# Optimization experiments

Measured on AMD Instinct MI355X. Metric: run time of the kernel, lower is better.

## Reference

```python
import jax, jax.numpy as jnp
import numpy as np
import itertools, functools, operator

NUM_RBF = 32
CUTOFF = 5.0
METRIC = (1, 1, 1)


def _count_bits(x):
    return bin(x).count("1")


def _sign_euclidean(a, b):
    a >>= 1
    s = 0
    while a:
        s += _count_bits(a & b)
        a >>= 1
    return 1 if (s & 1) == 0 else -1


def build_cayley(metric):
    """Dense [2^n, 2^n, 2^n] geometric multiplication (Cayley) table, shortlex blade order."""
    n = len(metric)
    blade_sets = itertools.chain.from_iterable(
        itertools.combinations([1 << i for i in range(n)], r) for r in range(n + 1)
    )
    index_to_bitmap = [functools.reduce(operator.or_, t, 0) for t in blade_sets]
    bitmap_to_index = {b: i for i, b in enumerate(index_to_bitmap)}
    N = 2 ** n
    cayley = np.zeros((N, N, N), dtype=np.float32)
    for i in range(N):
        bi = index_to_bitmap[i]
        for j in range(N):
            bj = index_to_bitmap[j]
            sign = _sign_euclidean(bi, bj)
            bm = bi & bj
            k = 0
            while bm:
                if bm & 1:
                    sign *= metric[k]
                k += 1
                bm >>= 1
            cayley[i, bitmap_to_index[bi ^ bj], j] = sign
    return cayley


CAYLEY = jnp.asarray(build_cayley(METRIC))  # [8,8,8], sparse +/-1 structure


def geometric_product(a, b):
    # torch: einsum('...i,ijk,...k->...j', a, cayley, b)
    return jnp.einsum('...i,ijk,...k->...j', a, CAYLEY, b)


def setup_inputs() -> dict:
    key = jax.random.key(0)
    k0, k1, k2, k3, k4, k5 = jax.random.split(key, 6)
    N, E, C = 50000, 800000, 16
    h = jax.random.normal(k0, (N, C, 8), jnp.float32)
    pos = jax.random.uniform(k1, (N, 3), jnp.float32) * 10.0
    edge_index = jax.random.randint(k2, (2, E), 0, N, jnp.int32)
    W_rbf = jax.random.normal(k3, (NUM_RBF, C), jnp.float32) / np.sqrt(NUM_RBF)
    W_out = jax.random.normal(k4, (C, C), jnp.float32) / np.sqrt(C)
    W_sgp = jax.random.normal(k5, (C, C), jnp.float32) / np.sqrt(C)
    return {"h": h, "pos": pos, "edge_index": edge_index,
            "W_rbf": W_rbf, "W_out": W_out, "W_sgp": W_sgp}


def reference(h, pos, edge_index, W_rbf, W_out, W_sgp):
    N, C, B = h.shape
    src, dst = edge_index[0], edge_index[1]

    # relative geometry
    rel = pos[dst] - pos[src]                                  # [E,3]
    dist = jnp.sqrt(jnp.sum(rel * rel, axis=-1) + 1e-12)       # [E]

    # embed unit relative vector as a grade-1 multivector (blades 1..3)
    rel_mv = jnp.zeros((rel.shape[0], 1, B), h.dtype)
    rel_mv = rel_mv.at[:, 0, 1:4].set(rel / dist[:, None])     # [E,1,8]

    # radial weights: gaussian smearing -> linear -> cosine cutoff envelope
    mus = jnp.linspace(0.0, CUTOFF, NUM_RBF, dtype=h.dtype)
    gamma = (NUM_RBF / CUTOFF) ** 2
    rbf = jnp.exp(-gamma * (dist[:, None] - mus) ** 2)         # [E,32]
    env = 0.5 * (jnp.cos(jnp.pi * dist / CUTOFF) + 1.0) * (dist < CUTOFF)
    w_e = (rbf @ W_rbf) * env[:, None]                          # [E,C]

    # equivariant messages: geometric product against edge multivector
    msg = geometric_product(h[src], rel_mv) * w_e[..., None]   # [E,C,8]
    agg = jax.ops.segment_sum(msg, dst, num_segments=N)        # [N,C,8]

    # MVLinear channel mixing (shared across blades)
    out = jnp.einsum('nci,co->noi', agg, W_out)                # [N,C,8]

    # MACE-style higher-order: steerable geometric product self-interaction
    q = jnp.einsum('nci,co->noi', h, W_sgp)                    # [N,C,8]
    return out + geometric_product(out, q)
```

## Files before the change

### kernel.cpp

```cpp
#include <hip/hip_runtime.h>

#define CUTOFF 5.0f
#define GAMMA 40.96f
#define MU_STEP 0.16129032f
#define INV_MU 6.2f
#define PI_F 3.14159265358979f
#define MAXDEG 64


__global__ __launch_bounds__(256) void k_fill_direct(
    const float* __restrict__ pos, const int* __restrict__ ei,
    int* __restrict__ deg, int* __restrict__ rec, int E)
{
    int e = blockIdx.x * 256 + threadIdx.x;
    if (e >= E) return;
    int src = ei[e], dst = ei[E + e];
    float dx = pos[dst*3+0] - pos[src*3+0];
    float dy = pos[dst*3+1] - pos[src*3+1];
    float dz = pos[dst*3+2] - pos[src*3+2];
    float d = sqrtf(dx*dx + dy*dy + dz*dz + 1e-12f);
    if (d < CUTOFF) {
        int slot = atomicAdd(&deg[dst], 1);
        if (slot < MAXDEG) rec[dst*MAXDEG + slot] = src;
    }
}

__global__ __launch_bounds__(256) void k_gather_finalize(
    const float* __restrict__ h, const float* __restrict__ pos,
    const int* __restrict__ rec, const int* __restrict__ deg,
    const float* __restrict__ Wrbf, const float* __restrict__ Wout,
    const float* __restrict__ Wsgp, float* __restrict__ out, int N)
{
    __shared__ float s_wr[512];
    __shared__ float s_Wout[256];
    __shared__ float s_Wsgp[256];
    __shared__ float s_agg[16*132];
    __shared__ float s_h[16*132];

    const int t  = threadIdx.x;
    const int nl = t >> 4;
    const int c  = t & 15;
    const int lane  = t & 63;
    const int gbase = lane & 48;
    const long long nodeBase = (long long)blockIdx.x * 16;
    const long long n = nodeBase + nl;

    s_wr[t]       = Wrbf[t];
    s_wr[t + 256] = Wrbf[t + 256];
    s_Wout[t] = Wout[t];
    s_Wsgp[t] = Wsgp[t];

    for (int idx = t; idx < 512; idx += 256) {
        int nn = idx >> 5;
        int r  = idx & 31;
        long long node = nodeBase + nn;
        float4 vh = make_float4(0,0,0,0);
        if (node < N) vh = *(const float4*)(h + node*128 + (long long)r*4);
        *(float4*)(&s_h[nn*132 + r*4]) = vh;
    }
    __syncthreads();

    float m0=0,m1=0,m2=0,m3=0,m4=0,m5=0,m6=0,m7=0;
    if (n < N) {
        const float px = pos[n*3+0], py = pos[n*3+1], pz = pos[n*3+2];
        const int start = (int)n * MAXDEG;
        const int dg    = min(deg[n], MAXDEG);
        for (int base = 0; base < dg; base += 2) {
            const int i1ok = (base + 1 < dg) ? 1 : 0;
            const int s0 = rec[start + base];
            const int s1 = rec[start + base + i1ok];

            const float4* hp0 = (const float4*)(h + (((long long)s0*16 + c) << 3));
            const float4* hp1 = (const float4*)(h + (((long long)s1*16 + c) << 3));
            const float4 A0 = hp0[0], B0 = hp0[1];
            const float4 A1 = hp1[0], B1 = hp1[1];

            const float dx0 = px - pos[s0*3+0];
            const float dy0 = py - pos[s0*3+1];
            const float dz0 = pz - pos[s0*3+2];
            const float dx1 = px - pos[s1*3+0];
            const float dy1 = py - pos[s1*3+1];
            const float dz1 = pz - pos[s1*3+2];

            const float d0 = sqrtf(dx0*dx0 + dy0*dy0 + dz0*dz0 + 1e-12f);
            const float d1 = sqrtf(dx1*dx1 + dy1*dy1 + dz1*dz1 + 1e-12f);
            const float inv0 = 1.0f / d0, inv1 = 1.0f / d1;
            const float ux0 = dx0*inv0, uy0 = dy0*inv0, uz0 = dz0*inv0;
            const float ux1 = dx1*inv1, uy1 = dy1*inv1, uz1 = dz1*inv1;
            const float env0 = 0.5f * (__cosf(PI_F * d0 * (1.0f/CUTOFF)) + 1.0f);
            const float env1 = 0.5f * (__cosf(PI_F * d1 * (1.0f/CUTOFF)) + 1.0f);

            const int kl0 = min(max(0, __float2int_rn(d0 * INV_MU) - 3), 25);
            const int kl1 = min(max(0, __float2int_rn(d1 * INV_MU) - 3), 25);

            const int   sel   = c >> 3;
            const float dsel  = sel ? d1 : d0;
            const int   klsel = sel ? kl1 : kl0;
            const float xx = dsel - MU_STEP * (float)(klsel + (c & 7));
            const float ee = __expf(-GAMMA * xx * xx);

            float w0 = 0.0f, w1 = 0.0f;
            #pragma unroll
            for (int j = 0; j < 7; ++j) {
                const float e0 = __shfl(ee, gbase + j);
                const float e1 = __shfl(ee, gbase + 8 + j);
                w0 += e0 * s_wr[(kl0 + j)*16 + c];
                w1 += e1 * s_wr[(kl1 + j)*16 + c];
            }
            w0 *= env0;
            w1 *= env1 * (float)i1ok;

            m0 += (A0.y*ux0 + A0.z*uy0 + A0.w*uz0) * w0 + (A1.y*ux1 + A1.z*uy1 + A1.w*uz1) * w1;
            m1 += (A0.x*ux0 + B0.x*uy0 + B0.y*uz0) * w0 + (A1.x*ux1 + B1.x*uy1 + B1.y*uz1) * w1;
            m2 += (A0.x*uy0 - B0.x*ux0 + B0.z*uz0) * w0 + (A1.x*uy1 - B1.x*ux1 + B1.z*uz1) * w1;
            m3 += (A0.x*uz0 - B0.y*ux0 - B0.z*uy0) * w0 + (A1.x*uz1 - B1.y*ux1 - B1.z*uy1) * w1;
            m4 += (A0.y*uy0 - A0.z*ux0 + B0.w*uz0) * w0 + (A1.y*uy1 - A1.z*ux1 + B1.w*uz1) * w1;
            m5 += (A0.y*uz0 - A0.w*ux0 - B0.w*uy0) * w0 + (A1.y*uz1 - A1.w*ux1 - B1.w*uy1) * w1;
            m6 += (A0.z*uz0 - A0.w*uy0 + B0.w*ux0) * w0 + (A1.z*uz1 - A1.w*uy1 + B1.w*ux1) * w1;
            m7 += (B0.z*ux0 - B0.y*uy0 + B0.x*uz0) * w0 + (B1.z*ux1 - B1.y*uy1 + B1.x*uz1) * w1;
        }
    }

    __syncthreads();
    float* ag = &s_agg[nl*132 + c*8];
    *(float4*)(ag)     = make_float4(m0, m1, m2, m3);
    *(float4*)(ag + 4) = make_float4(m4, m5, m6, m7);
    __syncthreads();

    const int o = c;
    const float* A = &s_agg[nl*132];
    const float* H = &s_h[nl*132];

    float o0=0,o1=0,o2=0,o3=0,o4=0,o5=0,o6=0,o7=0;
    float q0=0,q1=0,q2=0,q3=0,q4=0,q5=0,q6=0,q7=0;
    #pragma unroll
    for (int cc = 0; cc < 16; ++cc) {
        const float wo = s_Wout[cc*16 + o];
        const float ws = s_Wsgp[cc*16 + o];
        const float* a  = A + cc*8;
        const float* hh = H + cc*8;
        o0 += a[0]*wo; o1 += a[1]*wo; o2 += a[2]*wo; o3 += a[3]*wo;
        o4 += a[4]*wo; o5 += a[5]*wo; o6 += a[6]*wo; o7 += a[7]*wo;
        q0 += hh[0]*ws; q1 += hh[1]*ws; q2 += hh[2]*ws; q3 += hh[3]*ws;
        q4 += hh[4]*ws; q5 += hh[5]*ws; q6 += hh[6]*ws; q7 += hh[7]*ws;
    }

    const float r0 = o0 + (o0*q0 + o1*q1 + o2*q2 + o3*q3 - o4*q4 - o5*q5 - o6*q6 - o7*q7);
    const float r1 = o1 + (o0*q1 + o1*q0 - o2*q4 - o3*q5 + o4*q2 + o5*q3 - o6*q7 - o7*q6);
    const float r2 = o2 + (o0*q2 + o1*q4 + o2*q0 - o3*q6 - o4*q1 + o5*q7 + o6*q3 + o7*q5);
    const float r3 = o3 + (o0*q3 + o1*q5 + o2*q6 + o3*q0 - o4*q7 - o5*q1 - o6*q2 - o7*q4);
    const float r4 = o4 + (o0*q4 + o1*q2 - o2*q1 + o3*q7 + o4*q0 - o5*q6 + o6*q5 + o7*q3);
    const float r5 = o5 + (o0*q5 + o1*q3 - o2*q7 - o3*q1 + o4*q6 + o5*q0 - o6*q4 - o7*q2);
    const float r6 = o6 + (o0*q6 + o1*q7 + o2*q3 - o3*q2 - o4*q5 + o5*q4 + o6*q0 + o7*q1);
    const float r7 = o7 + (o0*q7 + o1*q6 - o2*q5 + o3*q4 + o4*q3 - o5*q2 + o6*q1 + o7*q0);

    if (n < N) {
        float* op = out + (n*16 + o)*8;
        *(float4*)(op)     = make_float4(r0, r1, r2, r3);
        *(float4*)(op + 4) = make_float4(r4, r5, r6, r7);
    }
}

extern "C" void kernel_launch(void* const* d_in, const int* in_sizes, int n_in,
                              void* d_out, int out_size, void* d_ws, size_t ws_size,
                              hipStream_t stream) {
    const float* h    = (const float*)d_in[0];
    const float* pos  = (const float*)d_in[1];
    const int*   ei   = (const int*)d_in[2];
    const float* Wrbf = (const float*)d_in[3];
    const float* Wout = (const float*)d_in[4];
    const float* Wsgp = (const float*)d_in[5];
    float* out = (float*)d_out;

    const int N = in_sizes[0] / 128;
    const int E = in_sizes[2] / 2;

    int* deg = (int*)d_ws;
    int* rec = deg + N;

    hipMemsetAsync(deg, 0, (size_t)N * sizeof(int), stream);

    const int eBlocks = (E + 255) / 256;
    k_fill_direct<<<eBlocks, 256, 0, stream>>>(pos, ei, deg, rec, E);

    const int gBlocks = (N + 15) / 16;
    k_gather_finalize<<<gBlocks, 256, 0, stream>>>(
        h, pos, rec, deg, Wrbf, Wout, Wsgp, out, N);
}
```

Before: 149.2 us.

## Fuse memset, edge bucketing and node gather into one cooperative persistent kernel

Replaces the memset plus two kernel launches with a single cooperative kernel that zeroes degrees, buckets edges by destination, then processes node tiles in a persistent loop, with grid-wide syncs between phases. The aim is to remove launch overhead and inter-kernel gaps. The cutoff test now compares squared distance and skips the sqrt. In exchange it adds grid.sync costs, caps the grid at the occupancy limit (hardcoded 256 CUs), and loops tiles persistently.

```diff
diff --git a/kernel.cpp b/kernel.cpp
--- a/kernel.cpp
+++ b/kernel.cpp
@@ -1,163 +1,171 @@
 #include <hip/hip_runtime.h>
+#include <hip/hip_cooperative_groups.h>
+
+namespace cg = cooperative_groups;
 
 #define CUTOFF 5.0f
+#define CUTOFF2 25.0f
 #define GAMMA 40.96f
 #define MU_STEP 0.16129032f
 #define INV_MU 6.2f
 #define PI_F 3.14159265358979f
 #define MAXDEG 64
 
-
-__global__ __launch_bounds__(256) void k_fill_direct(
-    const float* __restrict__ pos, const int* __restrict__ ei,
-    int* __restrict__ deg, int* __restrict__ rec, int E)
+__global__ __launch_bounds__(256) void k_fused(
+    const float* __restrict__ h, const float* __restrict__ pos,
+    const int* __restrict__ ei, const float* __restrict__ Wrbf,
+    const float* __restrict__ Wout, const float* __restrict__ Wsgp,
+    float* __restrict__ out, int* __restrict__ deg, int* __restrict__ rec,
+    int N, int E, int tiles)
 {
-    int e = blockIdx.x * 256 + threadIdx.x;
-    if (e >= E) return;
-    int src = ei[e], dst = ei[E + e];
-    float dx = pos[dst*3+0] - pos[src*3+0];
-    float dy = pos[dst*3+1] - pos[src*3+1];
-    float dz = pos[dst*3+2] - pos[src*3+2];
-    float d = sqrtf(dx*dx + dy*dy + dz*dz + 1e-12f);
-    if (d < CUTOFF) {
-        int slot = atomicAdd(&deg[dst], 1);
-        if (slot < MAXDEG) rec[dst*MAXDEG + slot] = src;
-    }
-}
-
-__global__ __launch_bounds__(256) void k_gather_finalize(
-    const float* __restrict__ h, const float* __restrict__ pos,
-    const int* __restrict__ rec, const int* __restrict__ deg,
-    const float* __restrict__ Wrbf, const float* __restrict__ Wout,
-    const float* __restrict__ Wsgp, float* __restrict__ out, int N)
-{
+    cg::grid_group grid = cg::this_grid();
+
     __shared__ float s_wr[512];
     __shared__ float s_Wout[256];
     __shared__ float s_Wsgp[256];
     __shared__ float s_agg[16*132];
     __shared__ float s_h[16*132];
 
-    const int t  = threadIdx.x;
-    const int nl = t >> 4;
-    const int c  = t & 15;
+    const int t     = threadIdx.x;
+    const int nl    = t >> 4;
+    const int c     = t & 15;
     const int lane  = t & 63;
     const int gbase = lane & 48;
-    const long long nodeBase = (long long)blockIdx.x * 16;
-    const long long n = nodeBase + nl;
+    const int gstride = gridDim.x * 256;
 
     s_wr[t]       = Wrbf[t];
     s_wr[t + 256] = Wrbf[t + 256];
     s_Wout[t] = Wout[t];
     s_Wsgp[t] = Wsgp[t];
 
-    for (int idx = t; idx < 512; idx += 256) {
-        int nn = idx >> 5;
-        int r  = idx & 31;
-        long long node = nodeBase + nn;
-        float4 vh = make_float4(0,0,0,0);
-        if (node < N) vh = *(const float4*)(h + node*128 + (long long)r*4);
-        *(float4*)(&s_h[nn*132 + r*4]) = vh;
+    for (int i = blockIdx.x * 256 + t; i < N; i += gstride) deg[i] = 0;
+    grid.sync();
+
+    for (int e = blockIdx.x * 256 + t; e < E; e += gstride) {
+        int src = ei[e], dst = ei[E + e];
+        float dx = pos[dst*3+0] - pos[src*3+0];
+        float dy = pos[dst*3+1] - pos[src*3+1];
+        float dz = pos[dst*3+2] - pos[src*3+2];
+        float d2 = dx*dx + dy*dy + dz*dz;
+        if (d2 < CUTOFF2) {
+            int slot = atomicAdd(&deg[dst], 1);
+            if (slot < MAXDEG) rec[dst*MAXDEG + slot] = src;
+        }
     }
-    __syncthreads();
-
-    float m0=0,m1=0,m2=0,m3=0,m4=0,m5=0,m6=0,m7=0;
-    if (n < N) {
-        const float px = pos[n*3+0], py = pos[n*3+1], pz = pos[n*3+2];
-        const int start = (int)n * MAXDEG;
-        const int dg    = min(deg[n], MAXDEG);
-        for (int base = 0; base < dg; base += 2) {
-            const int i1ok = (base + 1 < dg) ? 1 : 0;
-            const int s0 = rec[start + base];
-            const int s1 = rec[start + base + i1ok];
-
-            const float4* hp0 = (const float4*)(h + (((long long)s0*16 + c) << 3));
-            const float4* hp1 = (const float4*)(h + (((long long)s1*16 + c) << 3));
-            const float4 A0 = hp0[0], B0 = hp0[1];
-            const float4 A1 = hp1[0], B1 = hp1[1];
-
-            const float dx0 = px - pos[s0*3+0];
-            const float dy0 = py - pos[s0*3+1];
-            const float dz0 = pz - pos[s0*3+2];
-            const float dx1 = px - pos[s1*3+0];
-            const float dy1 = py - pos[s1*3+1];
-            const float dz1 = pz - pos[s1*3+2];
-
-            const float d0 = sqrtf(dx0*dx0 + dy0*dy0 + dz0*dz0 + 1e-12f);
-            const float d1 = sqrtf(dx1*dx1 + dy1*dy1 + dz1*dz1 + 1e-12f);
-            const float inv0 = 1.0f / d0, inv1 = 1.0f / d1;
-            const float ux0 = dx0*inv0, uy0 = dy0*inv0, uz0 = dz0*inv0;
-            const float ux1 = dx1*inv1, uy1 = dy1*inv1, uz1 = dz1*inv1;
-            const float env0 = 0.5f * (__cosf(PI_F * d0 * (1.0f/CUTOFF)) + 1.0f);
-            const float env1 = 0.5f * (__cosf(PI_F * d1 * (1.0f/CUTOFF)) + 1.0f);
-
-            const int kl0 = min(max(0, __float2int_rn(d0 * INV_MU) - 3), 25);
-            const int kl1 = min(max(0, __float2int_rn(d1 * INV_MU) - 3), 25);
-
-            const int   sel   = c >> 3;
-            const float dsel  = sel ? d1 : d0;
-            const int   klsel = sel ? kl1 : kl0;
-            const float xx = dsel - MU_STEP * (float)(klsel + (c & 7));
-            const float ee = __expf(-GAMMA * xx * xx);
-
-            float w0 = 0.0f, w1 = 0.0f;
-            #pragma unroll
-            for (int j = 0; j < 7; ++j) {
-                const float e0 = __shfl(ee, gbase + j);
-                const float e1 = __shfl(ee, gbase + 8 + j);
-                w0 += e0 * s_wr[(kl0 + j)*16 + c];
-                w1 += e1 * s_wr[(kl1 + j)*16 + c];
+    grid.sync();
+
+    for (int tile = blockIdx.x; tile < tiles; tile += gridDim.x) {
+        const long long nodeBase = (long long)tile * 16;
+        const long long n = nodeBase + nl;
+
+        for (int idx = t; idx < 512; idx += 256) {
+            int nn = idx >> 5;
+            int r  = idx & 31;
+            long long node = nodeBase + nn;
+            float4 vh = make_float4(0,0,0,0);
+            if (node < N) vh = *(const float4*)(h + node*128 + (long long)r*4);
+            *(float4*)(&s_h[nn*132 + r*4]) = vh;
+        }
+        __syncthreads();
+
+        float m0=0,m1=0,m2=0,m3=0,m4=0,m5=0,m6=0,m7=0;
+        if (n < N) {
+            const float px = pos[n*3+0], py = pos[n*3+1], pz = pos[n*3+2];
+            const int start = (int)n * MAXDEG;
+            const int dg    = min(deg[n], MAXDEG);
+            for (int base = 0; base < dg; base += 2) {
+                const int i1ok = (base + 1 < dg) ? 1 : 0;
+                const int s0 = rec[start + base];
+                const int s1 = rec[start + base + i1ok];
+
+                const float4* hp0 = (const float4*)(h + (((long long)s0*16 + c) << 3));
+                const float4* hp1 = (const float4*)(h + (((long long)s1*16 + c) << 3));
+                const float4 A0 = hp0[0], B0 = hp0[1];
+                const float4 A1 = hp1[0], B1 = hp1[1];
+
+                const float dx0 = px - pos[s0*3+0];
+                const float dy0 = py - pos[s0*3+1];
+                const float dz0 = pz - pos[s0*3+2];
+                const float dx1 = px - pos[s1*3+0];
+                const float dy1 = py - pos[s1*3+1];
+                const float dz1 = pz - pos[s1*3+2];
+
+                const float d0 = sqrtf(dx0*dx0 + dy0*dy0 + dz0*dz0 + 1e-12f);
+                const float d1 = sqrtf(dx1*dx1 + dy1*dy1 + dz1*dz1 + 1e-12f);
+                const float inv0 = 1.0f / d0, inv1 = 1.0f / d1;
+                const float ux0 = dx0*inv0, uy0 = dy0*inv0, uz0 = dz0*inv0;
+                const float ux1 = dx1*inv1, uy1 = dy1*inv1, uz1 = dz1*inv1;
+                const float env0 = 0.5f * (__cosf(PI_F * d0 * (1.0f/CUTOFF)) + 1.0f);
+                const float env1 = 0.5f * (__cosf(PI_F * d1 * (1.0f/CUTOFF)) + 1.0f);
+
+                const int kl0 = min(max(0, __float2int_rn(d0 * INV_MU) - 3), 25);
+                const int kl1 = min(max(0, __float2int_rn(d1 * INV_MU) - 3), 25);
+                const int   sel   = c >> 3;
+                const float dsel  = sel ? d1 : d0;
+                const int   klsel = sel ? kl1 : kl0;
+                const float xx = dsel - MU_STEP * (float)(klsel + (c & 7));
+                const float ee = __expf(-GAMMA * xx * xx);
+
+                float w0 = 0.0f, w1 = 0.0f;
+                #pragma unroll
+                for (int j = 0; j < 7; ++j) {
+                    const float e0 = __shfl(ee, gbase + j);
+                    const float e1 = __shfl(ee, gbase + 8 + j);
+                    w0 += e0 * s_wr[(kl0 + j)*16 + c];
+                    w1 += e1 * s_wr[(kl1 + j)*16 + c];
+                }
+                w0 *= env0;
+                w1 *= env1 * (float)i1ok;
+
+                m0 += (A0.y*ux0 + A0.z*uy0 + A0.w*uz0) * w0 + (A1.y*ux1 + A1.z*uy1 + A1.w*uz1) * w1;
+                m1 += (A0.x*ux0 + B0.x*uy0 + B0.y*uz0) * w0 + (A1.x*ux1 + B1.x*uy1 + B1.y*uz1) * w1;
+                m2 += (A0.x*uy0 - B0.x*ux0 + B0.z*uz0) * w0 + (A1.x*uy1 - B1.x*ux1 + B1.z*uz1) * w1;
+                m3 += (A0.x*uz0 - B0.y*ux0 - B0.z*uy0) * w0 + (A1.x*uz1 - B1.y*ux1 - B1.z*uy1) * w1;
+                m4 += (A0.y*uy0 - A0.z*ux0 + B0.w*uz0) * w0 + (A1.y*uy1 - A1.z*ux1 + B1.w*uz1) * w1;
+                m5 += (A0.y*uz0 - A0.w*ux0 - B0.w*uy0) * w0 + (A1.y*uz1 - A1.w*ux1 - B1.w*uy1) * w1;
+                m6 += (A0.z*uz0 - A0.w*uy0 + B0.w*ux0) * w0 + (A1.z*uz1 - A1.w*uy1 + B1.w*ux1) * w1;
+                m7 += (B0.z*ux0 - B0.y*uy0 + B0.x*uz0) * w0 + (B1.z*ux1 - B1.y*uy1 + B1.x*uz1) * w1;
             }
-            w0 *= env0;
-            w1 *= env1 * (float)i1ok;
-
-            m0 += (A0.y*ux0 + A0.z*uy0 + A0.w*uz0) * w0 + (A1.y*ux1 + A1.z*uy1 + A1.w*uz1) * w1;
-            m1 += (A0.x*ux0 + B0.x*uy0 + B0.y*uz0) * w0 + (A1.x*ux1 + B1.x*uy1 + B1.y*uz1) * w1;
-            m2 += (A0.x*uy0 - B0.x*ux0 + B0.z*uz0) * w0 + (A1.x*uy1 - B1.x*ux1 + B1.z*uz1) * w1;
-            m3 += (A0.x*uz0 - B0.y*ux0 - B0.z*uy0) * w0 + (A1.x*uz1 - B1.y*ux1 - B1.z*uy1) * w1;
-            m4 += (A0.y*uy0 - A0.z*ux0 + B0.w*uz0) * w0 + (A1.y*uy1 - A1.z*ux1 + B1.w*uz1) * w1;
-            m5 += (A0.y*uz0 - A0.w*ux0 - B0.w*uy0) * w0 + (A1.y*uz1 - A1.w*ux1 - B1.w*uy1) * w1;
-            m6 += (A0.z*uz0 - A0.w*uy0 + B0.w*ux0) * w0 + (A1.z*uz1 - A1.w*uy1 + B1.w*ux1) * w1;
-            m7 += (B0.z*ux0 - B0.y*uy0 + B0.x*uz0) * w0 + (B1.z*ux1 - B1.y*uy1 + B1.x*uz1) * w1;
-        }
-    }
-
-    __syncthreads();
-    float* ag = &s_agg[nl*132 + c*8];
-    *(float4*)(ag)     = make_float4(m0, m1, m2, m3);
-    *(float4*)(ag + 4) = make_float4(m4, m5, m6, m7);
-    __syncthreads();
-
-    const int o = c;
-    const float* A = &s_agg[nl*132];
-    const float* H = &s_h[nl*132];
-
-    float o0=0,o1=0,o2=0,o3=0,o4=0,o5=0,o6=0,o7=0;
-    float q0=0,q1=0,q2=0,q3=0,q4=0,q5=0,q6=0,q7=0;
-    #pragma unroll
-    for (int cc = 0; cc < 16; ++cc) {
-        const float wo = s_Wout[cc*16 + o];
-        const float ws = s_Wsgp[cc*16 + o];
-        const float* a  = A + cc*8;
-        const float* hh = H + cc*8;
-        o0 += a[0]*wo; o1 += a[1]*wo; o2 += a[2]*wo; o3 += a[3]*wo;
-        o4 += a[4]*wo; o5 += a[5]*wo; o6 += a[6]*wo; o7 += a[7]*wo;
-        q0 += hh[0]*ws; q1 += hh[1]*ws; q2 += hh[2]*ws; q3 += hh[3]*ws;
-        q4 += hh[4]*ws; q5 += hh[5]*ws; q6 += hh[6]*ws; q7 += hh[7]*ws;
-    }
-
-    const float r0 = o0 + (o0*q0 + o1*q1 + o2*q2 + o3*q3 - o4*q4 - o5*q5 - o6*q6 - o7*q7);
-    const float r1 = o1 + (o0*q1 + o1*q0 - o2*q4 - o3*q5 + o4*q2 + o5*q3 - o6*q7 - o7*q6);
-    const float r2 = o2 + (o0*q2 + o1*q4 + o2*q0 - o3*q6 - o4*q1 + o5*q7 + o6*q3 + o7*q5);
-    const float r3 = o3 + (o0*q3 + o1*q5 + o2*q6 + o3*q0 - o4*q7 - o5*q1 - o6*q2 - o7*q4);
-    const float r4 = o4 + (o0*q4 + o1*q2 - o2*q1 + o3*q7 + o4*q0 - o5*q6 + o6*q5 + o7*q3);
-    const float r5 = o5 + (o0*q5 + o1*q3 - o2*q7 - o3*q1 + o4*q6 + o5*q0 - o6*q4 - o7*q2);
-    const float r6 = o6 + (o0*q6 + o1*q7 + o2*q3 - o3*q2 - o4*q5 + o5*q4 + o6*q0 + o7*q1);
-    const float r7 = o7 + (o0*q7 + o1*q6 - o2*q5 + o3*q4 + o4*q3 - o5*q2 + o6*q1 + o7*q0);
-
-    if (n < N) {
-        float* op = out + (n*16 + o)*8;
-        *(float4*)(op)     = make_float4(r0, r1, r2, r3);
-        *(float4*)(op + 4) = make_float4(r4, r5, r6, r7);
+        }
+
+        float* ag = &s_agg[nl*132 + c*8];
+        *(float4*)(ag)     = make_float4(m0, m1, m2, m3);
+        *(float4*)(ag + 4) = make_float4(m4, m5, m6, m7);
+        __syncthreads();
+
+        const int o = c;
+        const float* A = &s_agg[nl*132];
+        const float* H = &s_h[nl*132];
+
+        float o0=0,o1=0,o2=0,o3=0,o4=0,o5=0,o6=0,o7=0;
+        float q0=0,q1=0,q2=0,q3=0,q4=0,q5=0,q6=0,q7=0;
+        #pragma unroll
+        for (int cc = 0; cc < 16; ++cc) {
+            const float wo = s_Wout[cc*16 + o];
+            const float ws = s_Wsgp[cc*16 + o];
+            const float* a  = A + cc*8;
+            const float* hh = H + cc*8;
+            o0 += a[0]*wo; o1 += a[1]*wo; o2 += a[2]*wo; o3 += a[3]*wo;
+            o4 += a[4]*wo; o5 += a[5]*wo; o6 += a[6]*wo; o7 += a[7]*wo;
+            q0 += hh[0]*ws; q1 += hh[1]*ws; q2 += hh[2]*ws; q3 += hh[3]*ws;
+            q4 += hh[4]*ws; q5 += hh[5]*ws; q6 += hh[6]*ws; q7 += hh[7]*ws;
+        }
+
+        const float r0 = o0 + (o0*q0 + o1*q1 + o2*q2 + o3*q3 - o4*q4 - o5*q5 - o6*q6 - o7*q7);
+        const float r1 = o1 + (o0*q1 + o1*q0 - o2*q4 - o3*q5 + o4*q2 + o5*q3 - o6*q7 - o7*q6);
+        const float r2 = o2 + (o0*q2 + o1*q4 + o2*q0 - o3*q6 - o4*q1 + o5*q7 + o6*q3 + o7*q5);
+        const float r3 = o3 + (o0*q3 + o1*q5 + o2*q6 + o3*q0 - o4*q7 - o5*q1 - o6*q2 - o7*q4);
+        const float r4 = o4 + (o0*q4 + o1*q2 - o2*q1 + o3*q7 + o4*q0 - o5*q6 + o6*q5 + o7*q3);
+        const float r5 = o5 + (o0*q5 + o1*q3 - o2*q7 - o3*q1 + o4*q6 + o5*q0 - o6*q4 - o7*q2);
+        const float r6 = o6 + (o0*q6 + o1*q7 + o2*q3 - o3*q2 - o4*q5 + o5*q4 + o6*q0 + o7*q1);
+        const float r7 = o7 + (o0*q7 + o1*q6 - o2*q5 + o3*q4 + o4*q3 - o5*q2 + o6*q1 + o7*q0);
+
+        if (n < N) {
+            float* op = out + (n*16 + o)*8;
+            *(float4*)(op)     = make_float4(r0, r1, r2, r3);
+            *(float4*)(op + 4) = make_float4(r4, r5, r6, r7);
+        }
+        __syncthreads();
     }
 }
 
@@ -172,18 +180,21 @@
     const float* Wsgp = (const float*)d_in[5];
     float* out = (float*)d_out;
 
-    const int N = in_sizes[0] / 128;
-    const int E = in_sizes[2] / 2;
+    int N = in_sizes[0] / 128;
+    int E = in_sizes[2] / 2;
+    int tiles = (N + 15) / 16;
 
     int* deg = (int*)d_ws;
     int* rec = deg + N;
 
-    hipMemsetAsync(deg, 0, (size_t)N * sizeof(int), stream);
-
-    const int eBlocks = (E + 255) / 256;
-    k_fill_direct<<<eBlocks, 256, 0, stream>>>(pos, ei, deg, rec, E);
-
-    const int gBlocks = (N + 15) / 16;
-    k_gather_finalize<<<gBlocks, 256, 0, stream>>>(
-        h, pos, rec, deg, Wrbf, Wout, Wsgp, out, N);
+    int blocksPerCU = 0;
+    hipOccupancyMaxActiveBlocksPerMultiprocessor(&blocksPerCU, k_fused, 256, 0);
+    if (blocksPerCU < 1) blocksPerCU = 1;
+    int grid = blocksPerCU * 256;
+
+    void* args[] = { (void*)&h, (void*)&pos, (void*)&ei, (void*)&Wrbf,
+                     (void*)&Wout, (void*)&Wsgp, (void*)&out,
+                     (void*)&deg, (void*)&rec, (void*)&N, (void*)&E, (void*)&tiles };
+    hipLaunchCooperativeKernel((const void*)k_fused, dim3(grid), dim3(256),
+                               args, 0, stream);
 }
```

Measured after the change: 271.9 us. 82.2% more time.

## Split each node's edge loop across two half-groups and reduce with shuffles

Applied to the files above, without the earlier changes.

The gather kernel now gives each node 32 threads instead of 16. Each 16-lane half handles alternating edge pairs, and the partial sums are combined with an xor-shuffle before the channel-mixing finalize, which only the first 128 threads run. The aim is more memory-level parallelism in the latency-bound gather and a shorter serial edge loop per thread. The cost is twice as many blocks and half the threads idle during finalize. The fill kernel also compares squared distance against the squared cutoff to avoid a sqrt.

```diff
diff --git a/kernel.cpp b/kernel.cpp
--- a/kernel.cpp
+++ b/kernel.cpp
@@ -1,6 +1,7 @@
 #include <hip/hip_runtime.h>
 
 #define CUTOFF 5.0f
+#define CUTOFF2 25.0f
 #define GAMMA 40.96f
 #define MU_STEP 0.16129032f
 #define INV_MU 6.2f
@@ -18,8 +19,8 @@
     float dx = pos[dst*3+0] - pos[src*3+0];
     float dy = pos[dst*3+1] - pos[src*3+1];
     float dz = pos[dst*3+2] - pos[src*3+2];
-    float d = sqrtf(dx*dx + dy*dy + dz*dz + 1e-12f);
-    if (d < CUTOFF) {
+    float d2 = dx*dx + dy*dy + dz*dz;
+    if (d2 < CUTOFF2) {
         int slot = atomicAdd(&deg[dst], 1);
         if (slot < MAXDEG) rec[dst*MAXDEG + slot] = src;
     }
@@ -34,15 +35,16 @@
     __shared__ float s_wr[512];
     __shared__ float s_Wout[256];
     __shared__ float s_Wsgp[256];
-    __shared__ float s_agg[16*132];
-    __shared__ float s_h[16*132];
+    __shared__ float s_agg[8*132];
+    __shared__ float s_h[8*132];
 
     const int t  = threadIdx.x;
-    const int nl = t >> 4;
+    const int nl = t >> 5;
+    const int s  = (t >> 4) & 1;
     const int c  = t & 15;
     const int lane  = t & 63;
     const int gbase = lane & 48;
-    const long long nodeBase = (long long)blockIdx.x * 16;
+    const long long nodeBase = (long long)blockIdx.x * 8;
     const long long n = nodeBase + nl;
 
     s_wr[t]       = Wrbf[t];
@@ -50,9 +52,8 @@
     s_Wout[t] = Wout[t];
     s_Wsgp[t] = Wsgp[t];
 
-    for (int idx = t; idx < 512; idx += 256) {
-        int nn = idx >> 5;
-        int r  = idx & 31;
+    {
+        int nn = t >> 5, r = t & 31;
         long long node = nodeBase + nn;
         float4 vh = make_float4(0,0,0,0);
         if (node < N) vh = *(const float4*)(h + node*128 + (long long)r*4);
@@ -65,7 +66,7 @@
         const float px = pos[n*3+0], py = pos[n*3+1], pz = pos[n*3+2];
         const int start = (int)n * MAXDEG;
         const int dg    = min(deg[n], MAXDEG);
-        for (int base = 0; base < dg; base += 2) {
+        for (int base = 2*s; base < dg; base += 4) {
             const int i1ok = (base + 1 < dg) ? 1 : 0;
             const int s0 = rec[start + base];
             const int s1 = rec[start + base + i1ok];
@@ -121,43 +122,53 @@
         }
     }
 
+    m0 += __shfl_xor(m0, 16); m1 += __shfl_xor(m1, 16);
+    m2 += __shfl_xor(m2, 16); m3 += __shfl_xor(m3, 16);
+    m4 += __shfl_xor(m4, 16); m5 += __shfl_xor(m5, 16);
+    m6 += __shfl_xor(m6, 16); m7 += __shfl_xor(m7, 16);
+
+    if (s == 0) {
+        float* ag = &s_agg[nl*132 + c*8];
+        *(float4*)(ag)     = make_float4(m0, m1, m2, m3);
+        *(float4*)(ag + 4) = make_float4(m4, m5, m6, m7);
+    }
     __syncthreads();
-    float* ag = &s_agg[nl*132 + c*8];
-    *(float4*)(ag)     = make_float4(m0, m1, m2, m3);
-    *(float4*)(ag + 4) = make_float4(m4, m5, m6, m7);
-    __syncthreads();
-
-    const int o = c;
-    const float* A = &s_agg[nl*132];
-    const float* H = &s_h[nl*132];
-
-    float o0=0,o1=0,o2=0,o3=0,o4=0,o5=0,o6=0,o7=0;
-    float q0=0,q1=0,q2=0,q3=0,q4=0,q5=0,q6=0,q7=0;
-    #pragma unroll
-    for (int cc = 0; cc < 16; ++cc) {
-        const float wo = s_Wout[cc*16 + o];
-        const float ws = s_Wsgp[cc*16 + o];
-        const float* a  = A + cc*8;
-        const float* hh = H + cc*8;
-        o0 += a[0]*wo; o1 += a[1]*wo; o2 += a[2]*wo; o3 += a[3]*wo;
-        o4 += a[4]*wo; o5 += a[5]*wo; o6 += a[6]*wo; o7 += a[7]*wo;
-        q0 += hh[0]*ws; q1 += hh[1]*ws; q2 += hh[2]*ws; q3 += hh[3]*ws;
-        q4 += hh[4]*ws; q5 += hh[5]*ws; q6 += hh[6]*ws; q7 += hh[7]*ws;
-    }
-
-    const float r0 = o0 + (o0*q0 + o1*q1 + o2*q2 + o3*q3 - o4*q4 - o5*q5 - o6*q6 - o7*q7);
-    const float r1 = o1 + (o0*q1 + o1*q0 - o2*q4 - o3*q5 + o4*q2 + o5*q3 - o6*q7 - o7*q6);
-    const float r2 = o2 + (o0*q2 + o1*q4 + o2*q0 - o3*q6 - o4*q1 + o5*q7 + o6*q3 + o7*q5);
-    const float r3 = o3 + (o0*q3 + o1*q5 + o2*q6 + o3*q0 - o4*q7 - o5*q1 - o6*q2 - o7*q4);
-    const float r4 = o4 + (o0*q4 + o1*q2 - o2*q1 + o3*q7 + o4*q0 - o5*q6 + o6*q5 + o7*q3);
-    const float r5 = o5 + (o0*q5 + o1*q3 - o2*q7 - o3*q1 + o4*q6 + o5*q0 - o6*q4 - o7*q2);
-    const float r6 = o6 + (o0*q6 + o1*q7 + o2*q3 - o3*q2 - o4*q5 + o5*q4 + o6*q0 + o7*q1);
-    const float r7 = o7 + (o0*q7 + o1*q6 - o2*q5 + o3*q4 + o4*q3 - o5*q2 + o6*q1 + o7*q0);
-
-    if (n < N) {
-        float* op = out + (n*16 + o)*8;
-        *(float4*)(op)     = make_float4(r0, r1, r2, r3);
-        *(float4*)(op + 4) = make_float4(r4, r5, r6, r7);
+
+    if (t < 128) {
+        const int n2 = t >> 4;
+        const int o  = t & 15;
+        const float* A = &s_agg[n2*132];
+        const float* H = &s_h[n2*132];
+
+        float o0=0,o1=0,o2=0,o3=0,o4=0,o5=0,o6=0,o7=0;
+        float q0=0,q1=0,q2=0,q3=0,q4=0,q5=0,q6=0,q7=0;
+        #pragma unroll
+        for (int cc = 0; cc < 16; ++cc) {
+            const float wo = s_Wout[cc*16 + o];
+            const float ws = s_Wsgp[cc*16 + o];
+            const float* a  = A + cc*8;
+            const float* hh = H + cc*8;
+            o0 += a[0]*wo; o1 += a[1]*wo; o2 += a[2]*wo; o3 += a[3]*wo;
+            o4 += a[4]*wo; o5 += a[5]*wo; o6 += a[6]*wo; o7 += a[7]*wo;
+            q0 += hh[0]*ws; q1 += hh[1]*ws; q2 += hh[2]*ws; q3 += hh[3]*ws;
+            q4 += hh[4]*ws; q5 += hh[5]*ws; q6 += hh[6]*ws; q7 += hh[7]*ws;
+        }
+
+        const float r0 = o0 + (o0*q0 + o1*q1 + o2*q2 + o3*q3 - o4*q4 - o5*q5 - o6*q6 - o7*q7);
+        const float r1 = o1 + (o0*q1 + o1*q0 - o2*q4 - o3*q5 + o4*q2 + o5*q3 - o6*q7 - o7*q6);
+        const float r2 = o2 + (o0*q2 + o1*q4 + o2*q0 - o3*q6 - o4*q1 + o5*q7 + o6*q3 + o7*q5);
+        const float r3 = o3 + (o0*q3 + o1*q5 + o2*q6 + o3*q0 - o4*q7 - o5*q1 - o6*q2 - o7*q4);
+        const float r4 = o4 + (o0*q4 + o1*q2 - o2*q1 + o3*q7 + o4*q0 - o5*q6 + o6*q5 + o7*q3);
+        const float r5 = o5 + (o0*q5 + o1*q3 - o2*q7 - o3*q1 + o4*q6 + o5*q0 - o6*q4 - o7*q2);
+        const float r6 = o6 + (o0*q6 + o1*q7 + o2*q3 - o3*q2 - o4*q5 + o5*q4 + o6*q0 + o7*q1);
+        const float r7 = o7 + (o0*q7 + o1*q6 - o2*q5 + o3*q4 + o4*q3 - o5*q2 + o6*q1 + o7*q0);
+
+        const long long nn = nodeBase + n2;
+        if (nn < N) {
+            float* op = out + (nn*16 + o)*8;
+            *(float4*)(op)     = make_float4(r0, r1, r2, r3);
+            *(float4*)(op + 4) = make_float4(r4, r5, r6, r7);
+        }
     }
 }
 
@@ -183,7 +194,7 @@
     const int eBlocks = (E + 255) / 256;
     k_fill_direct<<<eBlocks, 256, 0, stream>>>(pos, ei, deg, rec, E);
 
-    const int gBlocks = (N + 15) / 16;
+    const int gBlocks = (N + 7) / 8;
     k_gather_finalize<<<gBlocks, 256, 0, stream>>>(
         h, pos, rec, deg, Wrbf, Wout, Wsgp, out, N);
 }
```

After: 166.5 us. 11.5% more time.
